# Kernel optimization log

Hardware: AMD Instinct MI355X
Metric: run time of the kernel (lower is better)

Reference implementation:

```python
import math
import jax, jax.numpy as jnp
import numpy as np

B, S, HID, NH = 2, 2048, 2048, 16
HD = HID // NH          # 128
QKD = HD // 2           # 64
BASE = 10000.0
LAYER_ID = 1
LAMBDA_INIT = 0.8 - 0.6 * math.exp(-0.3 * LAYER_ID)
EPS = 1e-6


def _rope_tables():
    i = np.arange(0, HD, 2, dtype=np.float32)
    theta = BASE ** (-i / HD)                      # [HD/2]
    pos = np.arange(S, dtype=np.float32)
    m_theta = np.outer(pos, theta)                 # [S, HD/2]
    cos = np.repeat(np.cos(m_theta), 2, axis=1)    # [S, HD]
    sin = np.repeat(np.sin(m_theta), 2, axis=1)
    return jnp.asarray(cos), jnp.asarray(sin)


def setup_inputs() -> dict:
    key = jax.random.key(0)
    ks = jax.random.split(key, 12)
    wstd = 0.02
    cos_emb, sin_emb = _rope_tables()
    return {
        "q": jax.random.normal(ks[0], (B, S, HID), jnp.float32),
        "k": jax.random.normal(ks[1], (B, S, HID), jnp.float32),
        "v": jax.random.normal(ks[2], (B, S, HID), jnp.float32),
        "Wq": jax.random.normal(ks[3], (HID, HID), jnp.float32) * wstd,
        "Wk": jax.random.normal(ks[4], (HID, HID), jnp.float32) * wstd,
        "Wv": jax.random.normal(ks[5], (HID, HID), jnp.float32) * wstd,
        "Wo": jax.random.normal(ks[6], (HID, HID), jnp.float32) * wstd,
        "lambda_q1": jax.random.normal(ks[7], (HD,), jnp.float32) * 0.1,
        "lambda_k1": jax.random.normal(ks[8], (HD,), jnp.float32) * 0.1,
        "lambda_q2": jax.random.normal(ks[9], (HD,), jnp.float32) * 0.1,
        "lambda_k2": jax.random.normal(ks[10], (HD,), jnp.float32) * 0.1,
        "gnorm_w": jnp.ones((HD,), jnp.float32),
        "cos_emb": cos_emb,
        "sin_emb": sin_emb,
        "mask": jnp.triu(jnp.ones((S, S), bool), 1),  # causal: True = masked
    }


def _apply_rope(x, cos_emb, sin_emb):
    # x: [B, 2, H, S, QKD]; tables sliced to [:S, :QKD] as in the torch code
    cos = cos_emb[:S, :QKD][None, None, None]
    sin = sin_emb[:S, :QKD][None, None, None]
    inv = jnp.stack((-x[..., 1::2], x[..., 0::2]), axis=-1).reshape(x.shape)
    return x * cos + inv * sin


def reference(q, k, v, Wq, Wk, Wv, Wo, lambda_q1, lambda_k1, lambda_q2,
              lambda_k2, gnorm_w, cos_emb, sin_emb, mask):
    lin = lambda x, W: jnp.einsum('bsi,oi->bso', x, W)  # torch Linear: x @ W.T
    qh = lin(q, Wq).reshape(B, S, NH, 2, QKD).transpose(0, 3, 2, 1, 4)  # [B,2,H,S,QKD]
    kh = lin(k, Wk).reshape(B, S, NH, 2, QKD).transpose(0, 3, 2, 1, 4)
    vh = lin(v, Wv).reshape(B, S, NH, HD).transpose(0, 2, 1, 3)          # [B,H,S,HD]
    qh = _apply_rope(qh, cos_emb, sin_emb)
    kh = _apply_rope(kh, cos_emb, sin_emb)

    scores = jnp.einsum('bghsd,bghtd->bghst', qh, kh) / math.sqrt(QKD)   # [B,2,H,S,S]
    scores = jnp.where(mask, jnp.finfo(jnp.float32).min, scores)

    lam1 = jnp.exp(jnp.sum(lambda_q1 * lambda_k1))
    lam2 = jnp.exp(jnp.sum(lambda_q2 * lambda_k2))
    lam = lam1 - lam2 + LAMBDA_INIT

    attn = jax.nn.softmax(scores[:, 0], axis=-1) - lam * jax.nn.softmax(scores[:, 1], axis=-1)
    out = jnp.einsum('bhst,bhtd->bhsd', attn, vh)                        # [B,H,S,HD]

    rms = out * jax.lax.rsqrt(jnp.mean(out * out, axis=-1, keepdims=True) + EPS) * gnorm_w
    out = (1.0 - LAMBDA_INIT) * rms
    out = out.transpose(0, 2, 1, 3).reshape(B, S, HID)
    return lin(out, Wo)
```

## Files before the change

kernel.cpp:

```cpp
#include <hip/hip_runtime.h>
#include <math.h>

#define BDIM 2
#define SDIM 2048
#define HIDD 2048
#define NHH 16
#define HDD 128
#define QKDD 64
#define MTOT (BDIM*SDIM)

constexpr float LAMBDA_INIT_F = 0.3555090675909693f;
constexpr float EPS_F = 1e-6f;
constexpr float SCALE_F = 0.125f;

typedef float f32x4 __attribute__((ext_vector_type(4)));
typedef short bf16x8 __attribute__((ext_vector_type(8)));
typedef short bf16x4 __attribute__((ext_vector_type(4)));

#define MFMA16(a, b, c) __builtin_amdgcn_mfma_f32_16x16x32_bf16((a), (b), (c), 0, 0, 0)

__device__ __forceinline__ short f2bf(float f) {
    unsigned u = __float_as_uint(f);
    u += 0x7FFFu + ((u >> 16) & 1u);
    return (short)(u >> 16);
}
__device__ __forceinline__ unsigned pk2(float a, float b) {
    return (unsigned)(unsigned short)f2bf(a) | ((unsigned)(unsigned short)f2bf(b) << 16);
}

__device__ __forceinline__ void gload_lds16(const void* g, void* l) {
    __builtin_amdgcn_global_load_lds(
        (const __attribute__((address_space(1))) void*)g,
        (__attribute__((address_space(3))) void*)l, 16, 0, 0);
}
__device__ __forceinline__ void waitv8() { asm volatile("s_waitcnt vmcnt(8)" ::: "memory"); }
__device__ __forceinline__ void waitv0() { asm volatile("s_waitcnt vmcnt(0)" ::: "memory"); }
__device__ __forceinline__ void waitl0() { asm volatile("s_waitcnt lgkmcnt(0)" ::: "memory"); }
#define SBAR()   __builtin_amdgcn_s_barrier()
#define SCHEDB() __builtin_amdgcn_sched_barrier(0)

__global__ void lambda_kernel(const float* __restrict__ lq1, const float* __restrict__ lk1,
                              const float* __restrict__ lq2, const float* __restrict__ lk2,
                              float* __restrict__ lam_out) {
    int l = threadIdx.x;
    float d1 = lq1[l] * lk1[l] + lq1[l + 64] * lk1[l + 64];
    float d2 = lq2[l] * lk2[l] + lq2[l + 64] * lk2[l + 64];
#pragma unroll
    for (int o = 32; o > 0; o >>= 1) {
        d1 += __shfl_down(d1, o);
        d2 += __shfl_down(d2, o);
    }
    if (l == 0) lam_out[0] = expf(d1) - expf(d2) + LAMBDA_INIT_F;
}

__global__ __launch_bounds__(256) void conv_x(const float* __restrict__ s0,
                                              const float* __restrict__ s1,
                                              const float* __restrict__ s2,
                                              short* __restrict__ dst, int n) {
    const float* src = (blockIdx.y == 0) ? s0 : (blockIdx.y == 1) ? s1 : s2;
    short* out = dst + (size_t)blockIdx.y * n;
    int i = (blockIdx.x * 256 + threadIdx.x) * 8;
    if (i >= n) return;
    float4 a = *(const float4*)&src[i];
    float4 b = *(const float4*)&src[i + 4];
    uint4 o;
    o.x = pk2(a.x, a.y); o.y = pk2(a.z, a.w);
    o.z = pk2(b.x, b.y); o.w = pk2(b.z, b.w);
    *(uint4*)&out[i] = o;
}
__global__ __launch_bounds__(256) void conv_w(const float* __restrict__ s0,
                                              const float* __restrict__ s1,
                                              const float* __restrict__ s2,
                                              const float* __restrict__ s3,
                                              short* __restrict__ dst, int n) {
    const float* src = (blockIdx.y == 0) ? s0 : (blockIdx.y == 1) ? s1
                     : (blockIdx.y == 2) ? s2 : s3;
    short* out = dst + (size_t)blockIdx.y * n;
    int i = (blockIdx.x * 256 + threadIdx.x) * 8;
    if (i >= n) return;
    float4 a = *(const float4*)&src[i];
    float4 b = *(const float4*)&src[i + 4];
    uint4 o;
    o.x = pk2(a.x, a.y); o.y = pk2(a.z, a.w);
    o.z = pk2(b.x, b.y); o.w = pk2(b.z, b.w);
    *(uint4*)&out[i] = o;
}

#define GK 2048

__device__ __forceinline__ void gemm_mainloop(
        const short* __restrict__ X, const short* __restrict__ W,
        short* As, short* Bs, f32x4 acc[4][4],
        int bm, int bn, int w, int l, int lq, int lg, int wr, int wc) {
    const int scol = (((l & 7) ^ (l >> 3)) << 3);
    const int rsw  = (lq & 7) << 3;
    const short* aS[4]; const short* bS[4];
#pragma unroll
    for (int i = 0; i < 4; ++i) {
        const int c = w * 4 + i;
        aS[i] = X + (size_t)(bm + c * 8 + (l >> 3)) * GK + scol;
        bS[i] = W + (size_t)(bn + c * 8 + (l >> 3)) * GK + scol;
    }
    const int dOff = (w * 4) * 512;

#pragma unroll
    for (int i = 0; i < 4; ++i) {
        gload_lds16(aS[i], As + dOff + i * 512);
        gload_lds16(bS[i], Bs + dOff + i * 512);
    }
#pragma unroll
    for (int i = 0; i < 4; ++i) {
        gload_lds16(aS[i] + 64, As + 8192 + dOff + i * 512);
        gload_lds16(bS[i] + 64, Bs + 8192 + dOff + i * 512);
    }
    waitv8();
    SBAR();

    for (int t = 0; t < 30; ++t) {
        const short* Ab = As + (t & 1) * 8192;
        const short* Bb = Bs + (t & 1) * 8192;
        bf16x8 a[4][2], b[4][2];
#pragma unroll
        for (int m = 0; m < 4; ++m)
#pragma unroll
            for (int kk = 0; kk < 2; ++kk)
                a[m][kk] = *(const bf16x8*)&Ab[(wr * 64 + m * 16 + lq) * 64 + ((kk * 32 + lg * 8) ^ rsw)];
#pragma unroll
        for (int n = 0; n < 4; ++n)
#pragma unroll
            for (int kk = 0; kk < 2; ++kk)
                b[n][kk] = *(const bf16x8*)&Bb[(wc * 64 + n * 16 + lq) * 64 + ((kk * 32 + lg * 8) ^ rsw)];
        waitl0(); SCHEDB();
        SBAR();
        {
            short* Ad = As + (t & 1) * 8192 + dOff;
            short* Bd = Bs + (t & 1) * 8192 + dOff;
            const short* aK = aS[0] + (t + 2) * 64;
            (void)aK;
#pragma unroll
            for (int i = 0; i < 4; ++i) {
                gload_lds16(aS[i] + (t + 2) * 64, Ad + i * 512);
                gload_lds16(bS[i] + (t + 2) * 64, Bd + i * 512);
            }
        }
        SCHEDB();
#pragma unroll
        for (int kk = 0; kk < 2; ++kk)
#pragma unroll
            for (int m = 0; m < 4; ++m)
#pragma unroll
                for (int n = 0; n < 4; ++n)
                    acc[m][n] = MFMA16(a[m][kk], b[n][kk], acc[m][n]);
        waitv8();
        SBAR();
    }
    {
        bf16x8 a[4][2], b[4][2];
#pragma unroll
        for (int m = 0; m < 4; ++m)
#pragma unroll
            for (int kk = 0; kk < 2; ++kk)
                a[m][kk] = *(const bf16x8*)&As[(wr * 64 + m * 16 + lq) * 64 + ((kk * 32 + lg * 8) ^ rsw)];
#pragma unroll
        for (int n = 0; n < 4; ++n)
#pragma unroll
            for (int kk = 0; kk < 2; ++kk)
                b[n][kk] = *(const bf16x8*)&Bs[(wc * 64 + n * 16 + lq) * 64 + ((kk * 32 + lg * 8) ^ rsw)];
        waitl0(); SCHEDB();
        SBAR();
#pragma unroll
        for (int kk = 0; kk < 2; ++kk)
#pragma unroll
            for (int m = 0; m < 4; ++m)
#pragma unroll
                for (int n = 0; n < 4; ++n)
                    acc[m][n] = MFMA16(a[m][kk], b[n][kk], acc[m][n]);
        waitv0();
        SBAR();
    }
    {
        bf16x8 a[4][2], b[4][2];
#pragma unroll
        for (int m = 0; m < 4; ++m)
#pragma unroll
            for (int kk = 0; kk < 2; ++kk)
                a[m][kk] = *(const bf16x8*)&As[8192 + (wr * 64 + m * 16 + lq) * 64 + ((kk * 32 + lg * 8) ^ rsw)];
#pragma unroll
        for (int n = 0; n < 4; ++n)
#pragma unroll
            for (int kk = 0; kk < 2; ++kk)
                b[n][kk] = *(const bf16x8*)&Bs[8192 + (wc * 64 + n * 16 + lq) * 64 + ((kk * 32 + lg * 8) ^ rsw)];
#pragma unroll
        for (int kk = 0; kk < 2; ++kk)
#pragma unroll
            for (int m = 0; m < 4; ++m)
#pragma unroll
                for (int n = 0; n < 4; ++n)
                    acc[m][n] = MFMA16(a[m][kk], b[n][kk], acc[m][n]);
    }
}

__global__ __launch_bounds__(256) void qkv_gemm(
        const short* __restrict__ Xq, const short* __restrict__ Xk, const short* __restrict__ Xv,
        const short* __restrict__ Wb, short* __restrict__ Qb, short* __restrict__ Kb,
        short* __restrict__ Vb, const float* __restrict__ cosE, const float* __restrict__ sinE) {
    __shared__ short As[2 * 128 * 64];
    __shared__ short Bs[2 * 128 * 64];
    const int tid = threadIdx.x;
    const int w = tid >> 6, l = tid & 63;
    const int lq = l & 15, lg = l >> 4;
    const int wr = w >> 1, wc = w & 1;
    const int bm = blockIdx.y * 128;
    const int bn = blockIdx.x * 128;
    const int z  = blockIdx.z;

    const short* X = (z == 0) ? Xq : (z == 1) ? Xk : Xv;
    const short* W = Wb + (size_t)z * HIDD * HIDD;
    short* Cb      = (z == 0) ? Qb : (z == 1) ? Kb : Vb;

    f32x4 acc[4][4] = {};
    gemm_mainloop(X, W, As, Bs, acc, bm, bn, w, l, lq, lg, wr, wc);

    const bool dorope = (z < 2);
#pragma unroll
    for (int m = 0; m < 4; ++m)
#pragma unroll
        for (int n = 0; n < 4; ++n) {
            const int row0 = bm + wr * 64 + m * 16 + lg * 4;
            const int col  = bn + wc * 64 + n * 16 + lq;
#pragma unroll
            for (int r = 0; r < 4; ++r) {
                float vv = acc[m][n][r];
                if (dorope) {
                    const int s  = (row0 + r) & (SDIM - 1);
                    const int c6 = col & 63;
                    const float cv = cosE[s * HDD + c6];
                    const float sv = sinE[s * HDD + c6];
                    const float p = __shfl_xor(vv, 1);
                    vv = (col & 1) ? vv * cv + p * sv : vv * cv - p * sv;
                }
                Cb[(size_t)(row0 + r) * HIDD + col] = f2bf(vv);
            }
        }
}

__global__ __launch_bounds__(256) void o_gemm(const short* __restrict__ Ab,
                                              const short* __restrict__ Bb,
                                              float* __restrict__ C) {
    __shared__ short As[2 * 128 * 64];
    __shared__ short Bs[2 * 128 * 64];
    const int tid = threadIdx.x;
    const int w = tid >> 6, l = tid & 63;
    const int lq = l & 15, lg = l >> 4;
    const int wr = w >> 1, wc = w & 1;
    const int bm = blockIdx.y * 128;
    const int bn = blockIdx.x * 128;

    f32x4 acc[4][4] = {};
    gemm_mainloop(Ab, Bb, As, Bs, acc, bm, bn, w, l, lq, lg, wr, wc);

#pragma unroll
    for (int m = 0; m < 4; ++m)
#pragma unroll
        for (int n = 0; n < 4; ++n) {
            const int row0 = bm + wr * 64 + m * 16 + lg * 4;
            const int col  = bn + wc * 64 + n * 16 + lq;
#pragma unroll
            for (int r = 0; r < 4; ++r)
                C[(size_t)(row0 + r) * HIDD + col] = acc[m][n][r];
        }
}

#define KVB 64

__device__ __forceinline__ bf16x8 pack_pa(const float p0[4], const float p1[4]) {
    union { unsigned u[4]; bf16x8 v; } r;
    r.u[0] = pk2(p0[0], p0[1]);
    r.u[1] = pk2(p0[2], p0[3]);
    r.u[2] = pk2(p1[0], p1[1]);
    r.u[3] = pk2(p1[2], p1[3]);
    return r.v;
}

__device__ __forceinline__ void softmax_step(
        f32x4 sc[4], float& M, float& L, f32x4 O[8], bf16x8 pa[2],
        int t0, int qg, int lg, bool domask) {
#pragma unroll
    for (int sub = 0; sub < 4; ++sub)
#pragma unroll
        for (int r = 0; r < 4; ++r) {
            float s = sc[sub][r] * SCALE_F;
            if (domask) {
                int key = t0 + sub * 16 + lg * 4 + r;
                s = (key <= qg) ? s : -1e30f;
            }
            sc[sub][r] = s;
        }
    float mx = -1e30f;
#pragma unroll
    for (int sub = 0; sub < 4; ++sub) {
        float a01 = fmaxf(sc[sub][0], sc[sub][1]);
        float a23 = fmaxf(sc[sub][2], sc[sub][3]);
        mx = fmaxf(mx, fmaxf(a01, a23));
    }
    mx = fmaxf(mx, __shfl_xor(mx, 16));
    mx = fmaxf(mx, __shfl_xor(mx, 32));
    if (__ballot(mx > M + 8.f)) {
        const float Mn = fmaxf(M, mx);
        const float a = __expf(M - Mn);
        M = Mn;
        L *= a;
        float ar[4];
#pragma unroll
        for (int r = 0; r < 4; ++r) ar[r] = __shfl(a, lg * 4 + r);
#pragma unroll
        for (int d = 0; d < 8; ++d) {
            O[d][0] *= ar[0]; O[d][1] *= ar[1]; O[d][2] *= ar[2]; O[d][3] *= ar[3];
        }
    }
    float p[4][4];
    float ps = 0.f;
#pragma unroll
    for (int sub = 0; sub < 4; ++sub) {
#pragma unroll
        for (int r = 0; r < 4; ++r) p[sub][r] = __expf(sc[sub][r] - M);
        ps += (p[sub][0] + p[sub][1]) + (p[sub][2] + p[sub][3]);
    }
    ps += __shfl_xor(ps, 16);
    ps += __shfl_xor(ps, 32);
    L += ps;
    pa[0] = pack_pa(p[0], p[1]);
    pa[1] = pack_pa(p[2], p[3]);
}

__global__ __launch_bounds__(256, 2) void flash_mfma(
        const short* __restrict__ Qb, const short* __restrict__ Kb,
        const short* __restrict__ Vb, const float* __restrict__ gnw,
        const float* __restrict__ lam_p, short* __restrict__ Hob) {
    __shared__ short Ksh[KVB * 128];
    __shared__ short VT[HDD * 72];

    const int tid = threadIdx.x;
    const int w  = tid >> 6;
    const int l  = tid & 63;
    const int lq = l & 15;
    const int lg = l >> 4;

    const int blk = blockIdx.x;
    const int bh  = blk & 31;
    const int bx  = 31 - (blk >> 5);
    const int b = bh >> 4, h = bh & 15;
    const int s0 = bx * 64;
    const float lam = lam_p[0];

    const int qg = s0 + w * 16 + lq;
    const short* qrow = Qb + ((size_t)(b * SDIM + qg)) * HIDD + h * HDD;
    bf16x8 qf[2][2];
#pragma unroll
    for (int br = 0; br < 2; ++br)
#pragma unroll
        for (int ks = 0; ks < 2; ++ks)
            qf[br][ks] = *(const bf16x8*)(qrow + br * 64 + ks * 32 + lg * 8);

    int kkey[4], kcol[4];
#pragma unroll
    for (int i = 0; i < 4; ++i) {
        kkey[i] = w * 16 + i * 4 + lg;
        kcol[i] = (lq * 8) ^ ((kkey[i] & 7) << 3);
    }
    const int kp = tid & 31, dq = tid >> 5;

    const short* Kbase = Kb + ((size_t)(b * SDIM)) * HIDD + h * HDD;
    const short* Vbase = Vb + ((size_t)(b * SDIM)) * HIDD + h * HDD;

    float M1 = -1e30f, M2 = -1e30f, L1 = 0.f, L2 = 0.f;
    f32x4 O1[8] = {}; f32x4 O2[8] = {};

    const int ntmax = bx + 1;
    const int qmin = s0 + w * 16;
    const int ntw = (qmin >> 6) + 1;

    for (int t = 0; t < ntmax; ++t) {
        const size_t trow = (size_t)t * KVB * HIDD;
        __syncthreads();
#pragma unroll
        for (int i = 0; i < 4; ++i)
            gload_lds16(Kbase + trow + (size_t)kkey[i] * HIDD + kcol[i],
                        &Ksh[w * 2048 + i * 512]);
        {
            const short* v0 = Vbase + trow + (size_t)(2 * kp) * HIDD + dq * 16;
            const short* v1 = v0 + HIDD;
            bf16x8 v00 = *(const bf16x8*)v0;
            bf16x8 v01 = *(const bf16x8*)(v0 + 8);
            bf16x8 v10 = *(const bf16x8*)v1;
            bf16x8 v11 = *(const bf16x8*)(v1 + 8);
#pragma unroll
            for (int j = 0; j < 8; ++j) {
                unsigned ua = (unsigned)(unsigned short)v00[j] |
                              ((unsigned)(unsigned short)v10[j] << 16);
                *(unsigned*)&VT[(dq * 16 + j) * 72 + 2 * kp] = ua;
                unsigned ub = (unsigned)(unsigned short)v01[j] |
                              ((unsigned)(unsigned short)v11[j] << 16);
                *(unsigned*)&VT[(dq * 16 + 8 + j) * 72 + 2 * kp] = ub;
            }
        }
        __syncthreads();
        if (t >= ntw) continue;

        f32x4 sc1[4] = {}; f32x4 sc2[4] = {};
        const int rsw = (lq & 7) << 3;
        __builtin_amdgcn_s_setprio(1);
#pragma unroll
        for (int sub = 0; sub < 4; ++sub) {
            const int rbase = (sub * 16 + lq) * 128;
            bf16x8 k00 = *(const bf16x8*)&Ksh[rbase + ((lg * 8) ^ rsw)];
            bf16x8 k01 = *(const bf16x8*)&Ksh[rbase + ((32 + lg * 8) ^ rsw)];
            bf16x8 k10 = *(const bf16x8*)&Ksh[rbase + ((64 + lg * 8) ^ rsw)];
            bf16x8 k11 = *(const bf16x8*)&Ksh[rbase + ((96 + lg * 8) ^ rsw)];
            sc1[sub] = MFMA16(k00, qf[0][0], sc1[sub]);
            sc1[sub] = MFMA16(k01, qf[0][1], sc1[sub]);
            sc2[sub] = MFMA16(k10, qf[1][0], sc2[sub]);
            sc2[sub] = MFMA16(k11, qf[1][1], sc2[sub]);
        }
        __builtin_amdgcn_s_setprio(0);
        const int t0 = t * KVB;
        const bool domask = (t0 + KVB - 1 > qmin);
        bf16x8 pa1[2], pa2[2];
        softmax_step(sc1, M1, L1, O1, pa1, t0, qg, lg, domask);
        softmax_step(sc2, M2, L2, O2, pa2, t0, qg, lg, domask);

        __builtin_amdgcn_s_setprio(1);
#pragma unroll
        for (int d0 = 0; d0 < 8; ++d0) {
            const short* vrow = &VT[(d0 * 16 + lq) * 72];
            bf16x4 a0 = *(const bf16x4*)&vrow[lg * 4];
            bf16x4 a1 = *(const bf16x4*)&vrow[16 + lg * 4];
            bf16x4 b0 = *(const bf16x4*)&vrow[32 + lg * 4];
            bf16x4 b1 = *(const bf16x4*)&vrow[48 + lg * 4];
            bf16x8 vb0 = __builtin_shufflevector(a0, a1, 0, 1, 2, 3, 4, 5, 6, 7);
            bf16x8 vb1 = __builtin_shufflevector(b0, b1, 0, 1, 2, 3, 4, 5, 6, 7);
            O1[d0] = MFMA16(pa1[0], vb0, O1[d0]);
            O1[d0] = MFMA16(pa1[1], vb1, O1[d0]);
            O2[d0] = MFMA16(pa2[0], vb0, O2[d0]);
            O2[d0] = MFMA16(pa2[1], vb1, O2[d0]);
        }
        __builtin_amdgcn_s_setprio(0);
    }

    const float inv1 = 1.f / L1;
    const float inv2 = lam / L2;
    float i1[4], i2[4];
#pragma unroll
    for (int r = 0; r < 4; ++r) {
        i1[r] = __shfl(inv1, lg * 4 + r);
        i2[r] = __shfl(inv2, lg * 4 + r);
    }
    float gn[8];
#pragma unroll
    for (int d = 0; d < 8; ++d) gn[d] = gnw[d * 16 + lq];
    float od[8][4];
    float ss[4] = {0.f, 0.f, 0.f, 0.f};
#pragma unroll
    for (int d = 0; d < 8; ++d)
#pragma unroll
        for (int r = 0; r < 4; ++r) {
            float o = O1[d][r] * i1[r] - O2[d][r] * i2[r];
            od[d][r] = o;
            ss[r] += o * o;
        }
#pragma unroll
    for (int r = 0; r < 4; ++r) {
        ss[r] += __shfl_xor(ss[r], 1);
        ss[r] += __shfl_xor(ss[r], 2);
        ss[r] += __shfl_xor(ss[r], 4);
        ss[r] += __shfl_xor(ss[r], 8);
    }
#pragma unroll
    for (int r = 0; r < 4; ++r) {
        const float scal = rsqrtf(ss[r] * (1.0f / HDD) + EPS_F) * (1.0f - LAMBDA_INIT_F);
        const size_t orow = ((size_t)(b * SDIM + s0 + w * 16 + lg * 4 + r)) * HIDD + h * HDD;
#pragma unroll
        for (int d = 0; d < 8; ++d)
            Hob[orow + d * 16 + lq] = f2bf(od[d][r] * scal * gn[d]);
    }
}

extern "C" void kernel_launch(void* const* d_in, const int* in_sizes, int n_in,
                              void* d_out, int out_size, void* d_ws, size_t ws_size,
                              hipStream_t stream) {
    const float* q   = (const float*)d_in[0];
    const float* k   = (const float*)d_in[1];
    const float* v   = (const float*)d_in[2];
    const float* Wq  = (const float*)d_in[3];
    const float* Wk  = (const float*)d_in[4];
    const float* Wv  = (const float*)d_in[5];
    const float* Wo  = (const float*)d_in[6];
    const float* lq1 = (const float*)d_in[7];
    const float* lk1 = (const float*)d_in[8];
    const float* lq2 = (const float*)d_in[9];
    const float* lk2 = (const float*)d_in[10];
    const float* gnw = (const float*)d_in[11];
    const float* cosE = (const float*)d_in[12];
    const float* sinE = (const float*)d_in[13];
    float* out = (float*)d_out;

    const size_t TEN = (size_t)BDIM * SDIM * HIDD;
    const int   WN  = HIDD * HIDD;

    short* wsS = (short*)d_ws;
    short* Qb   = wsS;
    short* Kb   = wsS + TEN;
    short* Vb   = wsS + 2 * TEN;
    short* xqkv = wsS + 3 * TEN;
    short* wb4  = wsS + 6 * TEN;
    float* lamp = (float*)(wsS + 6 * TEN + (size_t)4 * WN);
    short* Hob  = xqkv;

    lambda_kernel<<<1, 64, 0, stream>>>(lq1, lk1, lq2, lk2, lamp);

    dim3 gx((int)(TEN / 8 / 256), 3);
    conv_x<<<gx, 256, 0, stream>>>(q, k, v, xqkv, (int)TEN);
    dim3 gw(WN / 8 / 256, 4);
    conv_w<<<gw, 256, 0, stream>>>(Wq, Wk, Wv, Wo, wb4, WN);

    dim3 gq(HIDD / 128, MTOT / 128, 3);
    qkv_gemm<<<gq, 256, 0, stream>>>(xqkv, xqkv + TEN, xqkv + 2 * TEN, wb4,
                                     Qb, Kb, Vb, cosE, sinE);

    flash_mfma<<<(SDIM / 64) * BDIM * NHH, 256, 0, stream>>>(Qb, Kb, Vb, gnw, lamp, Hob);

    dim3 go(HIDD / 128, MTOT / 128);
    o_gemm<<<go, 256, 0, stream>>>(Hob, wb4 + (size_t)3 * WN, out);
}
```

Before: 314.8 us.

## Replace QKV GEMM with 256x256-tile, 512-thread, quarter-phase pipelined kernel

The QKV projection moves from 128x128 tiles with 256 threads to 256x256 tiles with 512 threads and a 128KB LDS double buffer. Each K-step is split into four sub-phases that interleave global-to-LDS loads with MFMA work, and MFMA priority is raised via s_setprio. The block index is swizzled so neighbouring blocks share X/W tiles in cache. This is meant to raise arithmetic intensity and overlap loads with compute, at the cost of one block per CU, only 384 blocks, and higher register pressure (128 accumulators per thread).

```diff
diff --git a/kernel.cpp b/kernel.cpp
--- a/kernel.cpp
+++ b/kernel.cpp
@@ -34,6 +34,7 @@
         (__attribute__((address_space(3))) void*)l, 16, 0, 0);
 }
 __device__ __forceinline__ void waitv8() { asm volatile("s_waitcnt vmcnt(8)" ::: "memory"); }
+__device__ __forceinline__ void waitv6() { asm volatile("s_waitcnt vmcnt(6)" ::: "memory"); }
 __device__ __forceinline__ void waitv0() { asm volatile("s_waitcnt vmcnt(0)" ::: "memory"); }
 __device__ __forceinline__ void waitl0() { asm volatile("s_waitcnt lgkmcnt(0)" ::: "memory"); }
 #define SBAR()   __builtin_amdgcn_s_barrier()
@@ -88,145 +89,117 @@
 
 #define GK 2048
 
-__device__ __forceinline__ void gemm_mainloop(
-        const short* __restrict__ X, const short* __restrict__ W,
-        short* As, short* Bs, f32x4 acc[4][4],
-        int bm, int bn, int w, int l, int lq, int lg, int wr, int wc) {
-    const int scol = (((l & 7) ^ (l >> 3)) << 3);
-    const int rsw  = (lq & 7) << 3;
-    const short* aS[4]; const short* bS[4];
-#pragma unroll
-    for (int i = 0; i < 4; ++i) {
-        const int c = w * 4 + i;
-        aS[i] = X + (size_t)(bm + c * 8 + (l >> 3)) * GK + scol;
-        bS[i] = W + (size_t)(bn + c * 8 + (l >> 3)) * GK + scol;
-    }
-    const int dOff = (w * 4) * 512;
-
-#pragma unroll
-    for (int i = 0; i < 4; ++i) {
-        gload_lds16(aS[i], As + dOff + i * 512);
-        gload_lds16(bS[i], Bs + dOff + i * 512);
-    }
-#pragma unroll
-    for (int i = 0; i < 4; ++i) {
-        gload_lds16(aS[i] + 64, As + 8192 + dOff + i * 512);
-        gload_lds16(bS[i] + 64, Bs + 8192 + dOff + i * 512);
-    }
-    waitv8();
-    SBAR();
-
-    for (int t = 0; t < 30; ++t) {
-        const short* Ab = As + (t & 1) * 8192;
-        const short* Bb = Bs + (t & 1) * 8192;
-        bf16x8 a[4][2], b[4][2];
-#pragma unroll
-        for (int m = 0; m < 4; ++m)
-#pragma unroll
-            for (int kk = 0; kk < 2; ++kk)
-                a[m][kk] = *(const bf16x8*)&Ab[(wr * 64 + m * 16 + lq) * 64 + ((kk * 32 + lg * 8) ^ rsw)];
-#pragma unroll
-        for (int n = 0; n < 4; ++n)
-#pragma unroll
-            for (int kk = 0; kk < 2; ++kk)
-                b[n][kk] = *(const bf16x8*)&Bb[(wc * 64 + n * 16 + lq) * 64 + ((kk * 32 + lg * 8) ^ rsw)];
-        waitl0(); SCHEDB();
-        SBAR();
-        {
-            short* Ad = As + (t & 1) * 8192 + dOff;
-            short* Bd = Bs + (t & 1) * 8192 + dOff;
-            const short* aK = aS[0] + (t + 2) * 64;
-            (void)aK;
-#pragma unroll
-            for (int i = 0; i < 4; ++i) {
-                gload_lds16(aS[i] + (t + 2) * 64, Ad + i * 512);
-                gload_lds16(bS[i] + (t + 2) * 64, Bd + i * 512);
-            }
-        }
-        SCHEDB();
-#pragma unroll
-        for (int kk = 0; kk < 2; ++kk)
-#pragma unroll
-            for (int m = 0; m < 4; ++m)
-#pragma unroll
-                for (int n = 0; n < 4; ++n)
-                    acc[m][n] = MFMA16(a[m][kk], b[n][kk], acc[m][n]);
-        waitv8();
-        SBAR();
-    }
-    {
-        bf16x8 a[4][2], b[4][2];
-#pragma unroll
-        for (int m = 0; m < 4; ++m)
-#pragma unroll
-            for (int kk = 0; kk < 2; ++kk)
-                a[m][kk] = *(const bf16x8*)&As[(wr * 64 + m * 16 + lq) * 64 + ((kk * 32 + lg * 8) ^ rsw)];
-#pragma unroll
-        for (int n = 0; n < 4; ++n)
-#pragma unroll
-            for (int kk = 0; kk < 2; ++kk)
-                b[n][kk] = *(const bf16x8*)&Bs[(wc * 64 + n * 16 + lq) * 64 + ((kk * 32 + lg * 8) ^ rsw)];
-        waitl0(); SCHEDB();
-        SBAR();
-#pragma unroll
-        for (int kk = 0; kk < 2; ++kk)
-#pragma unroll
-            for (int m = 0; m < 4; ++m)
-#pragma unroll
-                for (int n = 0; n < 4; ++n)
-                    acc[m][n] = MFMA16(a[m][kk], b[n][kk], acc[m][n]);
-        waitv0();
-        SBAR();
-    }
-    {
-        bf16x8 a[4][2], b[4][2];
-#pragma unroll
-        for (int m = 0; m < 4; ++m)
-#pragma unroll
-            for (int kk = 0; kk < 2; ++kk)
-                a[m][kk] = *(const bf16x8*)&As[8192 + (wr * 64 + m * 16 + lq) * 64 + ((kk * 32 + lg * 8) ^ rsw)];
-#pragma unroll
-        for (int n = 0; n < 4; ++n)
-#pragma unroll
-            for (int kk = 0; kk < 2; ++kk)
-                b[n][kk] = *(const bf16x8*)&Bs[8192 + (wc * 64 + n * 16 + lq) * 64 + ((kk * 32 + lg * 8) ^ rsw)];
-#pragma unroll
-        for (int kk = 0; kk < 2; ++kk)
-#pragma unroll
-            for (int m = 0; m < 4; ++m)
-#pragma unroll
-                for (int n = 0; n < 4; ++n)
-                    acc[m][n] = MFMA16(a[m][kk], b[n][kk], acc[m][n]);
-    }
-}
-
-__global__ __launch_bounds__(256) void qkv_gemm(
+
+#define STAGE_A(BUF, QM, K0) do {                                              \
+    _Pragma("unroll") for (int j = 0; j < 2; ++j)                              \
+        gload_lds16(X + (size_t)(bm + arow0[j] + (QM) * 64) * GK + (K0) + scol,\
+                    &lds[(BUF) * 16384 + adst0[j] + (QM) * 4096]);             \
+} while (0)
+
+#define STAGE_B(BUF, QN, K0) do {                                              \
+    _Pragma("unroll") for (int j = 0; j < 2; ++j)                              \
+        gload_lds16(W + (size_t)(bn + brow0[j] + (QN) * 32) * GK + (K0) + scol,\
+                    &lds[32768 + (BUF) * 16384 + bdst0[j] + (QN) * 2048]);     \
+} while (0)
+
+#define PHASE(BUF, QM, QN, STAGE, WAITC) do {                                  \
+    bf16x8 aF[4][2]; bf16x8 bF[2][2];                                          \
+    _Pragma("unroll") for (int mp = 0; mp < 4; ++mp)                           \
+        _Pragma("unroll") for (int kk = 0; kk < 2; ++kk)                       \
+            aF[mp][kk] = *(const bf16x8*)&lds[(BUF) * 16384 +                  \
+                (wr * 128 + (QM) * 64 + mp * 16 + lq) * 64 +                   \
+                ((kk * 32 + lg * 8) ^ rswl)];                                  \
+    _Pragma("unroll") for (int np = 0; np < 2; ++np)                           \
+        _Pragma("unroll") for (int kk = 0; kk < 2; ++kk)                       \
+            bF[np][kk] = *(const bf16x8*)&lds[32768 + (BUF) * 16384 +          \
+                (wc * 64 + (QN) * 32 + np * 16 + lq) * 64 +                    \
+                ((kk * 32 + lg * 8) ^ rswl)];                                  \
+    STAGE;                                                                     \
+    SBAR();                                                                    \
+    waitl0(); SCHEDB();                                                        \
+    __builtin_amdgcn_s_setprio(1);                                             \
+    _Pragma("unroll") for (int kk = 0; kk < 2; ++kk)                           \
+        _Pragma("unroll") for (int mp = 0; mp < 4; ++mp)                       \
+            _Pragma("unroll") for (int np = 0; np < 2; ++np)                   \
+                acc[(QM) * 4 + mp][(QN) * 2 + np] =                            \
+                    MFMA16(aF[mp][kk], bF[np][kk],                             \
+                           acc[(QM) * 4 + mp][(QN) * 2 + np]);                 \
+    __builtin_amdgcn_s_setprio(0);                                             \
+    WAITC;                                                                     \
+    SBAR();                                                                    \
+} while (0)
+
+__global__ __launch_bounds__(512, 1) void qkv_gemm256(
         const short* __restrict__ Xq, const short* __restrict__ Xk, const short* __restrict__ Xv,
         const short* __restrict__ Wb, short* __restrict__ Qb, short* __restrict__ Kb,
         short* __restrict__ Vb, const float* __restrict__ cosE, const float* __restrict__ sinE) {
-    __shared__ short As[2 * 128 * 64];
-    __shared__ short Bs[2 * 128 * 64];
+    __shared__ short lds[65536];
+
     const int tid = threadIdx.x;
     const int w = tid >> 6, l = tid & 63;
     const int lq = l & 15, lg = l >> 4;
-    const int wr = w >> 1, wc = w & 1;
-    const int bm = blockIdx.y * 128;
-    const int bn = blockIdx.x * 128;
-    const int z  = blockIdx.z;
+    const int wr = w >> 2, wc = w & 3;
+    const int rswl = (lq & 7) << 3;
+
+    const int bid = blockIdx.x;
+    const int swz = (bid & 7) * 48 + (bid >> 3);
+    const int z   = swz >> 7;
+    const int rr  = swz & 127;
+    const int by  = rr >> 3;
+    const int bx  = rr & 7;
+    const int bm = by * 256, bn = bx * 256;
 
     const short* X = (z == 0) ? Xq : (z == 1) ? Xk : Xv;
     const short* W = Wb + (size_t)z * HIDD * HIDD;
     short* Cb      = (z == 0) ? Qb : (z == 1) ? Kb : Vb;
 
-    f32x4 acc[4][4] = {};
-    gemm_mainloop(X, W, As, Bs, acc, bm, bn, w, l, lq, lg, wr, wc);
+    int arow0[2], brow0[2], adst0[2], bdst0[2];
+#pragma unroll
+    for (int j = 0; j < 2; ++j) {
+        const int c  = w * 2 + j;
+        const int aRS = (c >> 3) * 128 + (c & 7) * 8;
+        const int bRS = (c >> 2) * 64 + (c & 3) * 8;
+        arow0[j] = aRS + (l >> 3);
+        brow0[j] = bRS + (l >> 3);
+        adst0[j] = aRS * 64;
+        bdst0[j] = bRS * 64;
+    }
+    const int scol = ((l & 7) ^ (l >> 3)) * 8;
+
+    f32x4 acc[8][4] = {};
+
+    STAGE_A(0, 0, 0); STAGE_B(0, 0, 0);
+    STAGE_B(0, 1, 0); STAGE_A(0, 1, 0);
+    STAGE_A(1, 0, 64); STAGE_B(1, 0, 64);
+    waitv6(); SBAR();
+
+    for (int it = 0; it < 15; ++it) {
+        const int t  = 2 * it;
+        const int k1 = (t + 1) * 64, k2 = (t + 2) * 64, k3 = (t + 3) * 64;
+        PHASE(0, 0, 0, STAGE_B(1, 1, k1), (void)0);
+        PHASE(0, 0, 1, STAGE_A(1, 1, k1), waitv6());
+        PHASE(0, 1, 0, STAGE_A(0, 0, k2), (void)0);
+        PHASE(0, 1, 1, STAGE_B(0, 0, k2), waitv6());
+        PHASE(1, 0, 0, STAGE_B(0, 1, k2), (void)0);
+        PHASE(1, 0, 1, STAGE_A(0, 1, k2), waitv6());
+        PHASE(1, 1, 0, STAGE_A(1, 0, k3), (void)0);
+        PHASE(1, 1, 1, STAGE_B(1, 0, k3), waitv6());
+    }
+    PHASE(0, 0, 0, STAGE_B(1, 1, 31 * 64), (void)0);
+    PHASE(0, 0, 1, STAGE_A(1, 1, 31 * 64), waitv6());
+    PHASE(0, 1, 0, (void)0, (void)0);
+    PHASE(0, 1, 1, (void)0, waitv0());
+    PHASE(1, 0, 0, (void)0, (void)0);
+    PHASE(1, 0, 1, (void)0, (void)0);
+    PHASE(1, 1, 0, (void)0, (void)0);
+    PHASE(1, 1, 1, (void)0, (void)0);
 
     const bool dorope = (z < 2);
 #pragma unroll
-    for (int m = 0; m < 4; ++m)
+    for (int m = 0; m < 8; ++m)
 #pragma unroll
         for (int n = 0; n < 4; ++n) {
-            const int row0 = bm + wr * 64 + m * 16 + lg * 4;
+            const int row0 = bm + wr * 128 + m * 16 + lg * 4;
             const int col  = bn + wc * 64 + n * 16 + lq;
 #pragma unroll
             for (int r = 0; r < 4; ++r) {
@@ -242,6 +215,116 @@
                 Cb[(size_t)(row0 + r) * HIDD + col] = f2bf(vv);
             }
         }
+}
+
+__device__ __forceinline__ void gemm_mainloop(
+        const short* __restrict__ X, const short* __restrict__ W,
+        short* As, short* Bs, f32x4 acc[4][4],
+        int bm, int bn, int w, int l, int lq, int lg, int wr, int wc) {
+    const int scol = (((l & 7) ^ (l >> 3)) << 3);
+    const int rsw  = (lq & 7) << 3;
+    const short* aS[4]; const short* bS[4];
+#pragma unroll
+    for (int i = 0; i < 4; ++i) {
+        const int c = w * 4 + i;
+        aS[i] = X + (size_t)(bm + c * 8 + (l >> 3)) * GK + scol;
+        bS[i] = W + (size_t)(bn + c * 8 + (l >> 3)) * GK + scol;
+    }
+    const int dOff = (w * 4) * 512;
+
+#pragma unroll
+    for (int i = 0; i < 4; ++i) {
+        gload_lds16(aS[i], As + dOff + i * 512);
+        gload_lds16(bS[i], Bs + dOff + i * 512);
+    }
+#pragma unroll
+    for (int i = 0; i < 4; ++i) {
+        gload_lds16(aS[i] + 64, As + 8192 + dOff + i * 512);
+        gload_lds16(bS[i] + 64, Bs + 8192 + dOff + i * 512);
+    }
+    waitv8();
+    SBAR();
+
+    for (int t = 0; t < 30; ++t) {
+        const short* Ab = As + (t & 1) * 8192;
+        const short* Bb = Bs + (t & 1) * 8192;
+        bf16x8 a[4][2], b[4][2];
+#pragma unroll
+        for (int m = 0; m < 4; ++m)
+#pragma unroll
+            for (int kk = 0; kk < 2; ++kk)
+                a[m][kk] = *(const bf16x8*)&Ab[(wr * 64 + m * 16 + lq) * 64 + ((kk * 32 + lg * 8) ^ rsw)];
+#pragma unroll
+        for (int n = 0; n < 4; ++n)
+#pragma unroll
+            for (int kk = 0; kk < 2; ++kk)
+                b[n][kk] = *(const bf16x8*)&Bb[(wc * 64 + n * 16 + lq) * 64 + ((kk * 32 + lg * 8) ^ rsw)];
+        waitl0(); SCHEDB();
+        SBAR();
+        {
+            short* Ad = As + (t & 1) * 8192 + dOff;
+            short* Bd = Bs + (t & 1) * 8192 + dOff;
+#pragma unroll
+            for (int i = 0; i < 4; ++i) {
+                gload_lds16(aS[i] + (t + 2) * 64, Ad + i * 512);
+                gload_lds16(bS[i] + (t + 2) * 64, Bd + i * 512);
+            }
+        }
+        SCHEDB();
+#pragma unroll
+        for (int kk = 0; kk < 2; ++kk)
+#pragma unroll
+            for (int m = 0; m < 4; ++m)
+#pragma unroll
+                for (int n = 0; n < 4; ++n)
+                    acc[m][n] = MFMA16(a[m][kk], b[n][kk], acc[m][n]);
+        waitv8();
+        SBAR();
+    }
+    {
+        bf16x8 a[4][2], b[4][2];
+#pragma unroll
+        for (int m = 0; m < 4; ++m)
+#pragma unroll
+            for (int kk = 0; kk < 2; ++kk)
+                a[m][kk] = *(const bf16x8*)&As[(wr * 64 + m * 16 + lq) * 64 + ((kk * 32 + lg * 8) ^ rsw)];
+#pragma unroll
+        for (int n = 0; n < 4; ++n)
+#pragma unroll
+            for (int kk = 0; kk < 2; ++kk)
+                b[n][kk] = *(const bf16x8*)&Bs[(wc * 64 + n * 16 + lq) * 64 + ((kk * 32 + lg * 8) ^ rsw)];
+        waitl0(); SCHEDB();
+        SBAR();
+#pragma unroll
+        for (int kk = 0; kk < 2; ++kk)
+#pragma unroll
+            for (int m = 0; m < 4; ++m)
+#pragma unroll
+                for (int n = 0; n < 4; ++n)
+                    acc[m][n] = MFMA16(a[m][kk], b[n][kk], acc[m][n]);
+        waitv0();
+        SBAR();
+    }
+    {
+        bf16x8 a[4][2], b[4][2];
+#pragma unroll
+        for (int m = 0; m < 4; ++m)
+#pragma unroll
+            for (int kk = 0; kk < 2; ++kk)
+                a[m][kk] = *(const bf16x8*)&As[8192 + (wr * 64 + m * 16 + lq) * 64 + ((kk * 32 + lg * 8) ^ rsw)];
+#pragma unroll
+        for (int n = 0; n < 4; ++n)
+#pragma unroll
+            for (int kk = 0; kk < 2; ++kk)
+                b[n][kk] = *(const bf16x8*)&Bs[8192 + (wc * 64 + n * 16 + lq) * 64 + ((kk * 32 + lg * 8) ^ rsw)];
+#pragma unroll
+        for (int kk = 0; kk < 2; ++kk)
+#pragma unroll
+            for (int m = 0; m < 4; ++m)
+#pragma unroll
+                for (int n = 0; n < 4; ++n)
+                    acc[m][n] = MFMA16(a[m][kk], b[n][kk], acc[m][n]);
+    }
 }
 
 __global__ __launch_bounds__(256) void o_gemm(const short* __restrict__ Ab,
@@ -523,9 +606,8 @@
     dim3 gw(WN / 8 / 256, 4);
     conv_w<<<gw, 256, 0, stream>>>(Wq, Wk, Wv, Wo, wb4, WN);
 
-    dim3 gq(HIDD / 128, MTOT / 128, 3);
-    qkv_gemm<<<gq, 256, 0, stream>>>(xqkv, xqkv + TEN, xqkv + 2 * TEN, wb4,
-                                     Qb, Kb, Vb, cosE, sinE);
+    qkv_gemm256<<<384, 512, 0, stream>>>(xqkv, xqkv + TEN, xqkv + 2 * TEN, wb4,
+                                         Qb, Kb, Vb, cosE, sinE);
 
     flash_mfma<<<(SDIM / 64) * BDIM * NHH, 256, 0, stream>>>(Qb, Kb, Vb, gnw, lamp, Hob);
 
```

Measured after the change: 366.1 us. 1.16x slower.

## Double-buffer K/V tiles in flash attention to prefetch next tile during compute

Applied to the files above, without the earlier changes.

Adds two LDS buffers for the K tile and the transposed V tile. The next tile's K is loaded asynchronously into the spare buffer, and its V is loaded into registers while the current tile's QK and softmax run. The V values are written to LDS before the PV MFMAs, and there is one barrier per iteration instead of two. It also drops the per-warp early skip of fully masked tiles, so every warp computes all tiles up to the block's maximum and relies on masking. LDS use doubles and V prefetch raises register pressure, which may hurt occupancy at launch bounds (256, 2).

```diff
diff --git a/kernel.cpp b/kernel.cpp
--- a/kernel.cpp
+++ b/kernel.cpp
@@ -135,8 +135,6 @@
         {
             short* Ad = As + (t & 1) * 8192 + dOff;
             short* Bd = Bs + (t & 1) * 8192 + dOff;
-            const short* aK = aS[0] + (t + 2) * 64;
-            (void)aK;
 #pragma unroll
             for (int i = 0; i < 4; ++i) {
                 gload_lds16(aS[i] + (t + 2) * 64, Ad + i * 512);
@@ -337,8 +335,8 @@
         const short* __restrict__ Qb, const short* __restrict__ Kb,
         const short* __restrict__ Vb, const float* __restrict__ gnw,
         const float* __restrict__ lam_p, short* __restrict__ Hob) {
-    __shared__ short Ksh[KVB * 128];
-    __shared__ short VT[HDD * 72];
+    __shared__ short Ksh[2][KVB * 128];
+    __shared__ short VT[2][HDD * 72];
 
     const int tid = threadIdx.x;
     const int w  = tid >> 6;
@@ -377,46 +375,57 @@
     f32x4 O1[8] = {}; f32x4 O2[8] = {};
 
     const int ntmax = bx + 1;
-    const int qmin = s0 + w * 16;
-    const int ntw = (qmin >> 6) + 1;
+    const int rsw = (lq & 7) << 3;
+
+    {
+        const short* v0 = Vbase + (size_t)(2 * kp) * HIDD + dq * 16;
+        bf16x8 vr0 = *(const bf16x8*)v0;
+        bf16x8 vr1 = *(const bf16x8*)(v0 + 8);
+        bf16x8 vr2 = *(const bf16x8*)(v0 + HIDD);
+        bf16x8 vr3 = *(const bf16x8*)(v0 + HIDD + 8);
+#pragma unroll
+        for (int i = 0; i < 4; ++i)
+            gload_lds16(Kbase + (size_t)kkey[i] * HIDD + kcol[i],
+                        &Ksh[0][w * 2048 + i * 512]);
+#pragma unroll
+        for (int j = 0; j < 8; ++j) {
+            unsigned ua = (unsigned)(unsigned short)vr0[j] |
+                          ((unsigned)(unsigned short)vr2[j] << 16);
+            *(unsigned*)&VT[0][(dq * 16 + j) * 72 + 2 * kp] = ua;
+            unsigned ub = (unsigned)(unsigned short)vr1[j] |
+                          ((unsigned)(unsigned short)vr3[j] << 16);
+            *(unsigned*)&VT[0][(dq * 16 + 8 + j) * 72 + 2 * kp] = ub;
+        }
+        waitv0(); waitl0();
+        SBAR();
+    }
 
     for (int t = 0; t < ntmax; ++t) {
-        const size_t trow = (size_t)t * KVB * HIDD;
-        __syncthreads();
-#pragma unroll
-        for (int i = 0; i < 4; ++i)
-            gload_lds16(Kbase + trow + (size_t)kkey[i] * HIDD + kcol[i],
-                        &Ksh[w * 2048 + i * 512]);
-        {
+        const int c = t & 1;
+        const bool stage = (t + 1 < ntmax);
+        bf16x8 vr0, vr1, vr2, vr3;
+        if (stage) {
+            const size_t trow = (size_t)(t + 1) * KVB * HIDD;
             const short* v0 = Vbase + trow + (size_t)(2 * kp) * HIDD + dq * 16;
-            const short* v1 = v0 + HIDD;
-            bf16x8 v00 = *(const bf16x8*)v0;
-            bf16x8 v01 = *(const bf16x8*)(v0 + 8);
-            bf16x8 v10 = *(const bf16x8*)v1;
-            bf16x8 v11 = *(const bf16x8*)(v1 + 8);
-#pragma unroll
-            for (int j = 0; j < 8; ++j) {
-                unsigned ua = (unsigned)(unsigned short)v00[j] |
-                              ((unsigned)(unsigned short)v10[j] << 16);
-                *(unsigned*)&VT[(dq * 16 + j) * 72 + 2 * kp] = ua;
-                unsigned ub = (unsigned)(unsigned short)v01[j] |
-                              ((unsigned)(unsigned short)v11[j] << 16);
-                *(unsigned*)&VT[(dq * 16 + 8 + j) * 72 + 2 * kp] = ub;
-            }
-        }
-        __syncthreads();
-        if (t >= ntw) continue;
+            vr0 = *(const bf16x8*)v0;
+            vr1 = *(const bf16x8*)(v0 + 8);
+            vr2 = *(const bf16x8*)(v0 + HIDD);
+            vr3 = *(const bf16x8*)(v0 + HIDD + 8);
+#pragma unroll
+            for (int i = 0; i < 4; ++i)
+                gload_lds16(Kbase + trow + (size_t)kkey[i] * HIDD + kcol[i],
+                            &Ksh[c ^ 1][w * 2048 + i * 512]);
+        }
 
         f32x4 sc1[4] = {}; f32x4 sc2[4] = {};
-        const int rsw = (lq & 7) << 3;
         __builtin_amdgcn_s_setprio(1);
 #pragma unroll
         for (int sub = 0; sub < 4; ++sub) {
-            const int rbase = (sub * 16 + lq) * 128;
-            bf16x8 k00 = *(const bf16x8*)&Ksh[rbase + ((lg * 8) ^ rsw)];
-            bf16x8 k01 = *(const bf16x8*)&Ksh[rbase + ((32 + lg * 8) ^ rsw)];
-            bf16x8 k10 = *(const bf16x8*)&Ksh[rbase + ((64 + lg * 8) ^ rsw)];
-            bf16x8 k11 = *(const bf16x8*)&Ksh[rbase + ((96 + lg * 8) ^ rsw)];
+            const short* krow = &Ksh[c][(sub * 16 + lq) * 128];
+            bf16x8 k00 = *(const bf16x8*)&krow[(lg * 8) ^ rsw];
+            bf16x8 k01 = *(const bf16x8*)&krow[(32 + lg * 8) ^ rsw];
+            bf16x8 k10 = *(const bf16x8*)&krow[(64 + lg * 8) ^ rsw];
+            bf16x8 k11 = *(const bf16x8*)&krow[(96 + lg * 8) ^ rsw];
             sc1[sub] = MFMA16(k00, qf[0][0], sc1[sub]);
             sc1[sub] = MFMA16(k01, qf[0][1], sc1[sub]);
             sc2[sub] = MFMA16(k10, qf[1][0], sc2[sub]);
@@ -424,15 +433,27 @@
         }
         __builtin_amdgcn_s_setprio(0);
         const int t0 = t * KVB;
-        const bool domask = (t0 + KVB - 1 > qmin);
+        const bool domask = (t0 + KVB - 1 > s0 + w * 16);
         bf16x8 pa1[2], pa2[2];
         softmax_step(sc1, M1, L1, O1, pa1, t0, qg, lg, domask);
         softmax_step(sc2, M2, L2, O2, pa2, t0, qg, lg, domask);
 
+        if (stage) {
+#pragma unroll
+            for (int j = 0; j < 8; ++j) {
+                unsigned ua = (unsigned)(unsigned short)vr0[j] |
+                              ((unsigned)(unsigned short)vr2[j] << 16);
+                *(unsigned*)&VT[c ^ 1][(dq * 16 + j) * 72 + 2 * kp] = ua;
+                unsigned ub = (unsigned)(unsigned short)vr1[j] |
+                              ((unsigned)(unsigned short)vr3[j] << 16);
+                *(unsigned*)&VT[c ^ 1][(dq * 16 + 8 + j) * 72 + 2 * kp] = ub;
+            }
+        }
+
         __builtin_amdgcn_s_setprio(1);
 #pragma unroll
         for (int d0 = 0; d0 < 8; ++d0) {
-            const short* vrow = &VT[(d0 * 16 + lq) * 72];
+            const short* vrow = &VT[c][(d0 * 16 + lq) * 72];
             bf16x4 a0 = *(const bf16x4*)&vrow[lg * 4];
             bf16x4 a1 = *(const bf16x4*)&vrow[16 + lg * 4];
             bf16x4 b0 = *(const bf16x4*)&vrow[32 + lg * 4];
@@ -445,6 +466,10 @@
             O2[d0] = MFMA16(pa2[1], vb1, O2[d0]);
         }
         __builtin_amdgcn_s_setprio(0);
+
+        if (stage) waitv0();
+        waitl0();
+        SBAR();
     }
 
     const float inv1 = 1.f / L1;
```

After: 322.4 us. 2.4% more time.
